# Kernel tuning notes

Hardware: AMD Instinct MI355X
Metric: run time of the kernel (lower is better)

Reference implementation:

```python
import jax, jax.numpy as jnp
import numpy as np

N_QUBITS = 12
N_LAYERS = 2
PATCH = 16
NPS = 14  # patches per side for 224/16
N_PATCHES = NPS * NPS
SCALE = 1.0 / np.sqrt(N_QUBITS)


def _butterfly_gates(n):
    # Faithful replication of QuantumOrthogonalLayer.butterfly_circuit indexing:
    # param_idx increments even when the (idx1, idx2) pair is skipped.
    gates, pidx = [], 0
    n_bl = int(np.ceil(np.log2(n)))
    for layer in range(n_bl):
        stride = 2 ** layer
        for start in range(0, n - stride, 2 * stride):
            for off in range(stride):
                i1, i2 = start + off, start + off + stride
                if i1 < n and i2 < n:
                    gates.append((pidx, i1, i2))
                pidx += 1
    nppl = sum(2 ** (n_bl - 1 - i) * 2 ** i for i in range(n_bl))  # n_params() = 32
    return gates, nppl

GATES, NPPL = _butterfly_gates(N_QUBITS)

# Pauli-Z sign table: qubit 0 is the most-significant bit of the flattened state index.
_bits = (np.arange(2 ** N_QUBITS)[:, None] >> np.arange(N_QUBITS - 1, -1, -1)[None, :]) & 1
Z_SIGNS = jnp.asarray(1.0 - 2.0 * _bits, dtype=jnp.float32)  # (4096, 12)


def _rbs_u(theta):
    # 4x4 real unitary of RY(2t,w1); CNOT(w1,w2); RY(-2t,w1); CNOT(w1,w2)
    c, s = jnp.cos(theta), jnp.sin(theta)
    c2, s2, cs = c * c, s * s, c * s
    return jnp.stack([
        jnp.stack([c2, s2, -cs, cs]),
        jnp.stack([s2, c2, cs, -cs]),
        jnp.stack([cs, -cs, c2, s2]),
        jnp.stack([-cs, cs, s2, c2]),
    ])


def _apply_2q(state, U, i, j):
    # state: (P, 2, 2, ..., 2); apply U to qubit axes i, j
    st = jnp.moveaxis(state, (1 + i, 1 + j), (-2, -1))
    shp = st.shape
    st = st.reshape(shp[:-2] + (4,)) @ U.T
    return jnp.moveaxis(st.reshape(shp), (-2, -1), (1 + i, 1 + j))


@jax.checkpoint
def quantum_expvals(features, params):
    # features: (P, n_qubits) angles; params: (N_LAYERS * NPPL,)
    P = features.shape[0]
    half = 0.5 * features
    amp = jnp.stack([jnp.cos(half), jnp.sin(half)], axis=-1)  # (P, n, 2) RY(x)|0>
    state = jnp.ones((P, 1), features.dtype)
    for q in range(N_QUBITS):  # product-state angle encoding
        state = (state[:, :, None] * amp[:, q][:, None, :]).reshape(P, -1)
    state = state.reshape((P,) + (2,) * N_QUBITS)
    for l in range(N_LAYERS):
        base = l * NPPL
        for pidx, w1, w2 in GATES:
            state = _apply_2q(state, _rbs_u(params[base + pidx]), w1, w2)
    probs = state.reshape(P, -1) ** 2
    return probs @ Z_SIGNS  # (P, n_qubits) <Z_i>


def setup_inputs() -> dict:
    key = jax.random.key(0)
    ks = jax.random.split(key, 6)
    x = jax.random.normal(ks[0], (4, 3, 224, 224), dtype=jnp.float32)
    W_proj = jax.random.normal(ks[1], (N_QUBITS, PATCH * PATCH), dtype=jnp.float32) / np.sqrt(PATCH * PATCH)
    b_proj = jnp.zeros((N_QUBITS,), jnp.float32)
    q_params = 0.1 * jax.random.normal(ks[2], (N_LAYERS * NPPL,), dtype=jnp.float32)
    k_params = 0.1 * jax.random.normal(ks[3], (N_LAYERS * NPPL,), dtype=jnp.float32)
    v_params = 0.1 * jax.random.normal(ks[4], (N_LAYERS * NPPL,), dtype=jnp.float32)
    W_cls = jax.random.normal(ks[5], (1000, N_PATCHES * N_QUBITS), dtype=jnp.float32) / np.sqrt(N_PATCHES * N_QUBITS)
    b_cls = jnp.zeros((1000,), jnp.float32)
    return {"x": x, "W_proj": W_proj, "b_proj": b_proj, "q_params": q_params,
            "k_params": k_params, "v_params": v_params, "W_cls": W_cls, "b_cls": b_cls}


def reference(x, W_proj, b_proj, q_params, k_params, v_params, W_cls, b_cls):
    B = x.shape[0]
    xg = jnp.mean(x, axis=1)  # channel average -> (B, H, W)
    patches = xg.reshape(B, NPS, PATCH, NPS, PATCH).transpose(0, 1, 3, 2, 4)
    patches = patches.reshape(B, N_PATCHES, PATCH * PATCH)
    proj = patches @ W_proj.T + b_proj  # (B, n_patches, n_qubits)
    feats = proj.reshape(-1, N_QUBITS)
    Q = quantum_expvals(feats, q_params).reshape(B, N_PATCHES, N_QUBITS)
    K = quantum_expvals(feats, k_params).reshape(B, N_PATCHES, N_QUBITS)
    V = quantum_expvals(feats, v_params).reshape(B, N_PATCHES, N_QUBITS)
    attn = jax.nn.softmax(jnp.einsum('bqd,bkd->bqk', Q, K) * SCALE, axis=-1)
    out = jnp.einsum('bqk,bkd->bqd', attn, V)  # (B, n_patches, n_qubits)
    logits = out.reshape(B, -1) @ W_cls.T + b_cls
    return logits
```

## Files before the change

kernel.cpp:

```cpp
#include <hip/hip_runtime.h>
#include <math.h>

#define NQ        12
#define NPS       14
#define NPATCH    196
#define NB        4
#define NCLS      1000
#define FEATDIM   2352
#define SCALE_F   0.28867513459481287f

typedef float v2f __attribute__((ext_vector_type(2)));

constexpr int PRa[8][5] = {
    {2,3,0,1, 4},
    {2,3,4,5, 6},
    {2,3,5,6, 7},
    {2,3,0,4, 6},
    {2,3,8,9,10},
    {2,3,9,10,11},
    {2,3,0,8,10},
    {2,3,1,5, 9},
};
constexpr int PTa[8][7] = {
    {5,6,7,8,9,10,11},
    {7,0,1,8,9,10,11},
    {0,1,4,8,9,10,11},
    {8,9,10,1,5,7,11},
    {4,0,1,5,6,7,11},
    {0,1,8,5,6,7,4},
    {1,5,9,6,7,11,4},
    {6,0,11,7,8,10,4},
};
constexpr bool BARa[8] = {false,false,false,false,true,false,false,true};

constexpr int cwgt(int X, int q) {
    for (int k = 0; k < 5; ++k) if (PRa[X][k] == q) return 1 << k;
    for (int m = 0; m < 7; ++m) if (PTa[X][m] == q) return 36 << m;
    return 0;
}
constexpr int rimmB(int X, int Y, int a) {
    int s = 0;
    for (int j = 0; j < 3; ++j)
        if ((a >> j) & 1) s += cwgt(X, PRa[Y][2 + j]);
    return s;
}

template<int TI>
__device__ __forceinline__ void relayoutB(v2f amp2[16], float* lds, int tid, int base) {
    constexpr int X = TI, Y = (TI + 1) & 7;
    float4* dst = (float4*)(lds + 36 * tid);
    #pragma unroll
    for (int k = 0; k < 8; ++k)
        dst[k] = make_float4(amp2[2*k][0], amp2[2*k][1], amp2[2*k+1][0], amp2[2*k+1][1]);
    if (BARa[TI]) __syncthreads();
    #pragma unroll
    for (int a = 0; a < 8; ++a) {
        float4 v = *(const float4*)(lds + base + rimmB(X, Y, a));
        amp2[2*a][0] = v.x; amp2[2*a][1] = v.y;
        amp2[2*a+1][0] = v.z; amp2[2*a+1][1] = v.w;
    }
    if (BARa[TI]) __syncthreads();
}

template<int MI, int MJ>
__device__ __forceinline__ void pk_gate(v2f a[16], float gc, float gs) {
    v2f H = {0.5f, 0.5f}, C = {gc, gc}, S = {gs, gs};
    #pragma unroll
    for (int m = 0; m < 16; ++m) {
        if (m & (MI | MJ)) continue;
        v2f a0 = a[m], a1 = a[m | MJ], a2 = a[m | MI], a3 = a[m | MI | MJ];
        v2f p  = a0 + a1, q  = a0 - a1;
        v2f p2 = a2 + a3, q2 = a2 - a3;
        v2f t1 = H * p  + C * q  - S * q2;
        v2f t2 = H * p2 + C * q2 + S * q;
        a[m]           = t1;
        a[m | MJ]      = p  - t1;
        a[m | MI]      = t2;
        a[m | MI | MJ] = p2 - t2;
    }
}

template<int MI, int MJ>
__device__ __forceinline__ void sc_gate(float* amp, float gc, float gs) {
    #pragma unroll
    for (int m = 0; m < 32; ++m) {
        if (m & (MI | MJ)) continue;
        float a0 = amp[m], a1 = amp[m | MJ], a2 = amp[m | MI], a3 = amp[m | MI | MJ];
        float p  = a0 + a1, q  = a0 - a1;
        float p2 = a2 + a3, q2 = a2 - a3;
        float t1 = 0.5f * p  + gc * q  - gs * q2;
        float t2 = 0.5f * p2 + gc * q2 + gs * q;
        amp[m]           = t1;
        amp[m | MJ]      = p  - t1;
        amp[m | MI]      = t2;
        amp[m | MI | MJ] = p2 - t2;
    }
}

template<int CTRL>
__device__ __forceinline__ float dppadd(float x) {
    int s = __builtin_amdgcn_update_dpp(0, __float_as_int(x), CTRL, 0xf, 0xf, true);
    return x + __int_as_float(s);
}
__device__ __forceinline__ float wave_sum(float x) {
    x = dppadd<0x111>(x);
    x = dppadd<0x112>(x);
    x = dppadd<0x114>(x);
    x = dppadd<0x118>(x);
    x = dppadd<0x142>(x);
    x = dppadd<0x143>(x);
    return x;
}

__global__ __launch_bounds__(128, 4) void qcirc_kernel(
    const float* __restrict__ x,
    const float* __restrict__ Wp,
    const float* __restrict__ bproj,
    const float* __restrict__ qp,
    const float* __restrict__ kp,
    const float* __restrict__ vp,
    float* __restrict__ qkv)
{
    __shared__ __align__(16) float lds[4608];
    __shared__ float chs[NQ], shs[NQ];
    __shared__ float gC[40], gS[40];
    __shared__ float red2[2][12];

    const int tid = threadIdx.x;
    const int p = blockIdx.x, b = blockIdx.y, c = blockIdx.z;
    const int bp = b * NPATCH + p;
    const float* params = (c == 0) ? qp : (c == 1) ? kp : vp;
    const int lane = tid & 63, wv = tid >> 6;

    float part[NQ];
    #pragma unroll
    for (int q = 0; q < NQ; ++q) part[q] = 0.0f;
    {
        int py = p / NPS, px = p % NPS;
        const float* xb = x + (size_t)b * 3 * 224 * 224;
        #pragma unroll
        for (int k = 0; k < 2; ++k) {
            int pix = tid + 128 * k;
            int off = (py * 16 + (pix >> 4)) * 224 + px * 16 + (pix & 15);
            float v = (xb[off] + xb[off + 50176] + xb[off + 100352]) * (1.0f / 3.0f);
            #pragma unroll
            for (int q = 0; q < NQ; ++q) part[q] += v * Wp[q * 256 + pix];
        }
    }
    if (tid < 40) {
        int l = tid / 20, g = tid - l * 20;
        float th = params[l * 32 + g];
        gC[tid] = 0.5f * cosf(2.0f * th);
        gS[tid] = 0.5f * sinf(2.0f * th);
    }
    #pragma unroll
    for (int q = 0; q < NQ; ++q) part[q] = wave_sum(part[q]);
    if (lane == 63) {
        #pragma unroll
        for (int q = 0; q < NQ; ++q) red2[wv][q] = part[q];
    }
    __syncthreads();
    if (tid < NQ) {
        float h = 0.5f * (red2[0][tid] + red2[1][tid] + bproj[tid]);
        chs[tid] = cosf(h); shs[tid] = sinf(h);
    }
    __syncthreads();

    int baseT[8];
    #pragma unroll
    for (int TI = 0; TI < 8; ++TI) {
        int Y = (TI + 1) & 7, s = 0;
        #pragma unroll
        for (int j = 0; j < 7; ++j)
            s += ((tid >> j) & 1) ? cwgt(TI, PTa[Y][j]) : 0;
        baseT[TI] = s;
    }

    v2f amp2[16];
    float* amp = (float*)amp2;
    {
        float hi = ((tid &  1) ? shs[5]  : chs[5])  *
                   ((tid &  2) ? shs[6]  : chs[6])  *
                   ((tid &  4) ? shs[7]  : chs[7])  *
                   ((tid &  8) ? shs[8]  : chs[8])  *
                   ((tid & 16) ? shs[9]  : chs[9])  *
                   ((tid & 32) ? shs[10] : chs[10]) *
                   ((tid & 64) ? shs[11] : chs[11]);
        float pA[8], pB[4];
        #pragma unroll
        for (int i = 0; i < 8; ++i)
            pA[i] = ((i & 1) ? shs[2] : chs[2]) * ((i & 2) ? shs[3] : chs[3]) *
                    ((i & 4) ? shs[0] : chs[0]);
        #pragma unroll
        for (int i = 0; i < 4; ++i)
            pB[i] = ((i & 1) ? shs[1] : chs[1]) * ((i & 2) ? shs[4] : chs[4]);
        #pragma unroll
        for (int r = 0; r < 32; ++r) amp[r] = pA[r & 7] * pB[r >> 3] * hi;
    }

    #pragma unroll 1
    for (int l = 0; l < 2; ++l) {
        const int bb = l * 20;
        pk_gate<2, 4>(amp2, gC[bb+0], gS[bb+0]);
        sc_gate<1, 2>(amp,  gC[bb+1], gS[bb+1]);
        sc_gate<4, 1>(amp,  gC[bb+6], gS[bb+6]);
        pk_gate<4, 1>(amp2, gC[bb+7], gS[bb+7]);
        relayoutB<0>(amp2, lds, tid, baseT[0]);
        pk_gate<2, 4>(amp2, gC[bb+2], gS[bb+2]);
        relayoutB<1>(amp2, lds, tid, baseT[1]);
        pk_gate<4, 8>(amp2, gC[bb+3],  gS[bb+3]);
        pk_gate<2, 8>(amp2, gC[bb+9],  gS[bb+9]);
        pk_gate<1, 8>(amp2, gC[bb+15], gS[bb+15]);
        relayoutB<2>(amp2, lds, tid, baseT[2]);
        pk_gate<4, 8>(amp2, gC[bb+8],  gS[bb+8]);
        pk_gate<2, 4>(amp2, gC[bb+12], gS[bb+12]);
        sc_gate<1,16>(amp,  gC[bb+14], gS[bb+14]);
        relayoutB<3>(amp2, lds, tid, baseT[3]);
        pk_gate<2, 4>(amp2, gC[bb+4], gS[bb+4]);
        relayoutB<4>(amp2, lds, tid, baseT[4]);
        pk_gate<4, 8>(amp2, gC[bb+5],  gS[bb+5]);
        pk_gate<2, 8>(amp2, gC[bb+11], gS[bb+11]);
        pk_gate<1, 8>(amp2, gC[bb+19], gS[bb+19]);
        relayoutB<5>(amp2, lds, tid, baseT[5]);
        pk_gate<4, 8>(amp2, gC[bb+10], gS[bb+10]);
        pk_gate<2, 4>(amp2, gC[bb+16], gS[bb+16]);
        sc_gate<1,16>(amp,  gC[bb+18], gS[bb+18]);
        relayoutB<6>(amp2, lds, tid, baseT[6]);
        pk_gate<2, 4>(amp2, gC[bb+13], gS[bb+13]);
        pk_gate<2, 8>(amp2, gC[bb+17], gS[bb+17]);
        if (l == 0) relayoutB<7>(amp2, lds, tid, baseT[7]);
    }

    float T, Sq2, Sq3, Sq1, Sq5, Sq9;
    {
        float t1[16]; Sq2 = 0.0f;
        #pragma unroll
        for (int i = 0; i < 16; ++i) {
            float e = amp[2*i] * amp[2*i], o = amp[2*i+1] * amp[2*i+1];
            t1[i] = e + o; Sq2 += e - o;
        }
        float t2[8]; Sq3 = 0.0f;
        #pragma unroll
        for (int i = 0; i < 8; ++i) { t2[i] = t1[2*i] + t1[2*i+1]; Sq3 += t1[2*i] - t1[2*i+1]; }
        float t3[4]; Sq1 = 0.0f;
        #pragma unroll
        for (int i = 0; i < 4; ++i) { t3[i] = t2[2*i] + t2[2*i+1]; Sq1 += t2[2*i] - t2[2*i+1]; }
        float t4[2]; Sq5 = 0.0f;
        #pragma unroll
        for (int i = 0; i < 2; ++i) { t4[i] = t3[2*i] + t3[2*i+1]; Sq5 += t3[2*i] - t3[2*i+1]; }
        T = t4[0] + t4[1]; Sq9 = t4[0] - t4[1];
    }
    float Vq6  = (tid &  1) ? -T : T;
    float Vq0  = (tid &  2) ? -T : T;
    float Vq11 = (tid &  4) ? -T : T;
    float Vq7  = (tid &  8) ? -T : T;
    float Vq8  = (tid & 16) ? -T : T;
    float Vq10 = (tid & 32) ? -T : T;
    T    = wave_sum(T);
    Vq6  = wave_sum(Vq6);  Vq0  = wave_sum(Vq0);  Vq11 = wave_sum(Vq11);
    Vq7  = wave_sum(Vq7);  Vq8  = wave_sum(Vq8);  Vq10 = wave_sum(Vq10);
    Sq2  = wave_sum(Sq2);  Sq3  = wave_sum(Sq3);  Sq1  = wave_sum(Sq1);
    Sq5  = wave_sum(Sq5);  Sq9  = wave_sum(Sq9);
    if (lane == 63) {
        red2[wv][0]  = Vq0;  red2[wv][1]  = Sq1;  red2[wv][2]  = Sq2;
        red2[wv][3]  = Sq3;  red2[wv][4]  = T;    red2[wv][5]  = Sq5;
        red2[wv][6]  = Vq6;  red2[wv][7]  = Vq7;  red2[wv][8]  = Vq8;
        red2[wv][9]  = Sq9;  red2[wv][10] = Vq10; red2[wv][11] = Vq11;
    }
    __syncthreads();
    if (tid < NQ) {
        float v1 = red2[1][tid];
        float s = red2[0][tid] + ((tid == 4) ? -v1 : v1);
        qkv[((size_t)c * (NB * NPATCH) + bp) * NQ + tid] = s;
    }
}

__global__ __launch_bounds__(256) void attn_kernel(
    const float* __restrict__ qkv,
    float* __restrict__ outb)
{
    int tid = threadIdx.x;
    int qp = blockIdx.x, b = blockIdx.y;
    const float* Q = qkv;
    const float* K = qkv + NB * NPATCH * NQ;
    const float* V = qkv + 2 * NB * NPATCH * NQ;

    __shared__ float redm[4], reds[4], redv[4][NQ];

    float4 q0 = ((const float4*)(Q + (b * NPATCH + qp) * NQ))[0];
    float4 q1 = ((const float4*)(Q + (b * NPATCH + qp) * NQ))[1];
    float4 q2 = ((const float4*)(Q + (b * NPATCH + qp) * NQ))[2];

    float score = -1e30f;
    float4 v0, v1, v2;
    if (tid < NPATCH) {
        const float4* K4 = (const float4*)(K + (b * NPATCH + tid) * NQ);
        float4 k0 = K4[0], k1 = K4[1], k2 = K4[2];
        float s = q0.x*k0.x + q0.y*k0.y + q0.z*k0.z + q0.w*k0.w
                + q1.x*k1.x + q1.y*k1.y + q1.z*k1.z + q1.w*k1.w
                + q2.x*k2.x + q2.y*k2.y + q2.z*k2.z + q2.w*k2.w;
        score = s * SCALE_F;
        const float4* V4 = (const float4*)(V + (b * NPATCH + tid) * NQ);
        v0 = V4[0]; v1 = V4[1]; v2 = V4[2];
    }
    float m = score;
    #pragma unroll
    for (int o = 32; o > 0; o >>= 1) m = fmaxf(m, __shfl_down(m, o));
    int lane = tid & 63, wv = tid >> 6;
    if (lane == 0) redm[wv] = m;
    __syncthreads();
    float maxv = fmaxf(fmaxf(redm[0], redm[1]), fmaxf(redm[2], redm[3]));

    float w = (tid < NPATCH) ? expf(score - maxv) : 0.0f;
    float sm = w;
    #pragma unroll
    for (int o = 32; o > 0; o >>= 1) sm += __shfl_down(sm, o);
    if (lane == 0) reds[wv] = sm;

    float part[NQ];
    #pragma unroll
    for (int d = 0; d < NQ; d++) part[d] = 0.0f;
    if (tid < NPATCH) {
        part[0] = w*v0.x; part[1] = w*v0.y; part[2]  = w*v0.z; part[3]  = w*v0.w;
        part[4] = w*v1.x; part[5] = w*v1.y; part[6]  = w*v1.z; part[7]  = w*v1.w;
        part[8] = w*v2.x; part[9] = w*v2.y; part[10] = w*v2.z; part[11] = w*v2.w;
    }
    #pragma unroll
    for (int d = 0; d < NQ; d++) {
        #pragma unroll
        for (int o = 32; o > 0; o >>= 1) part[d] += __shfl_down(part[d], o);
    }
    if (lane == 0) {
        #pragma unroll
        for (int d = 0; d < NQ; d++) redv[wv][d] = part[d];
    }
    __syncthreads();
    if (tid < NQ) {
        float sumv = reds[0] + reds[1] + reds[2] + reds[3];
        float s = redv[0][tid] + redv[1][tid] + redv[2][tid] + redv[3][tid];
        outb[(size_t)b * FEATDIM + qp * NQ + tid] = s / sumv;
    }
}

__global__ __launch_bounds__(256) void cls_kernel(
    const float* __restrict__ outb,
    const float* __restrict__ Wc,
    const float* __restrict__ bc,
    float* __restrict__ logits)
{
    int o = blockIdx.x, tid = threadIdx.x;
    float acc[NB] = {0.0f, 0.0f, 0.0f, 0.0f};
    const float4* w4 = (const float4*)(Wc + (size_t)o * FEATDIM);
    for (int j = tid; j < FEATDIM / 4; j += 256) {
        float4 w = w4[j];
        #pragma unroll
        for (int b = 0; b < NB; b++) {
            float4 ov = ((const float4*)(outb + (size_t)b * FEATDIM))[j];
            acc[b] += w.x*ov.x + w.y*ov.y + w.z*ov.z + w.w*ov.w;
        }
    }
    #pragma unroll
    for (int b = 0; b < NB; b++) {
        #pragma unroll
        for (int off = 32; off > 0; off >>= 1) acc[b] += __shfl_down(acc[b], off);
    }
    __shared__ float red[4][NB];
    int lane = tid & 63, wv = tid >> 6;
    if (lane == 0) {
        #pragma unroll
        for (int b = 0; b < NB; b++) red[wv][b] = acc[b];
    }
    __syncthreads();
    if (tid < NB) {
        float s = red[0][tid] + red[1][tid] + red[2][tid] + red[3][tid];
        logits[(size_t)tid * NCLS + o] = s + bc[o];
    }
}

extern "C" void kernel_launch(void* const* d_in, const int* in_sizes, int n_in,
                              void* d_out, int out_size, void* d_ws, size_t ws_size,
                              hipStream_t stream) {
    const float* x     = (const float*)d_in[0];
    const float* Wp    = (const float*)d_in[1];
    const float* bproj = (const float*)d_in[2];
    const float* qp    = (const float*)d_in[3];
    const float* kp    = (const float*)d_in[4];
    const float* vp    = (const float*)d_in[5];
    const float* Wc    = (const float*)d_in[6];
    const float* bc    = (const float*)d_in[7];
    float* logits = (float*)d_out;

    float* ws   = (float*)d_ws;
    float* qkv  = ws;
    float* outb = ws + 28224;

    qcirc_kernel<<<dim3(NPATCH, NB, 3), 128, 0, stream>>>(x, Wp, bproj, qp, kp, vp, qkv);
    attn_kernel <<<dim3(NPATCH, NB),    256, 0, stream>>>(qkv, outb);
    cls_kernel  <<<NCLS,                256, 0, stream>>>(outb, Wc, bc, logits);
}
```

Baseline: 116.5 us.

## Simulate Q, K, V circuits in one block sharing projection and interleaved stages

Merges the three per-parameter-set circuit blocks into one block per patch. The patch load and projection are now done once instead of three times, and the three state vectors are evolved together with their stages interleaved so each one's LDS relayout can overlap the others' gate math. The cost is three times the amplitude registers per thread, which removes the occupancy hint and may cause spills. The grid also shrinks to a third of its size, cutting parallelism to 784 blocks.

```diff
diff --git a/kernel.cpp b/kernel.cpp
--- a/kernel.cpp
+++ b/kernel.cpp
@@ -103,134 +103,34 @@
     return x + __int_as_float(s);
 }
 __device__ __forceinline__ float wave_sum(float x) {
-    x = dppadd<0x111>(x);
-    x = dppadd<0x112>(x);
-    x = dppadd<0x114>(x);
-    x = dppadd<0x118>(x);
-    x = dppadd<0x142>(x);
-    x = dppadd<0x143>(x);
+    x = dppadd<0x111>(x); x = dppadd<0x112>(x); x = dppadd<0x114>(x);
+    x = dppadd<0x118>(x); x = dppadd<0x142>(x); x = dppadd<0x143>(x);
     return x;
 }
 
-__global__ __launch_bounds__(128, 4) void qcirc_kernel(
-    const float* __restrict__ x,
-    const float* __restrict__ Wp,
-    const float* __restrict__ bproj,
-    const float* __restrict__ qp,
-    const float* __restrict__ kp,
-    const float* __restrict__ vp,
-    float* __restrict__ qkv)
-{
-    __shared__ __align__(16) float lds[4608];
-    __shared__ float chs[NQ], shs[NQ];
-    __shared__ float gC[40], gS[40];
-    __shared__ float red2[2][12];
-
-    const int tid = threadIdx.x;
-    const int p = blockIdx.x, b = blockIdx.y, c = blockIdx.z;
-    const int bp = b * NPATCH + p;
-    const float* params = (c == 0) ? qp : (c == 1) ? kp : vp;
-    const int lane = tid & 63, wv = tid >> 6;
-
-    float part[NQ];
-    #pragma unroll
-    for (int q = 0; q < NQ; ++q) part[q] = 0.0f;
-    {
-        int py = p / NPS, px = p % NPS;
-        const float* xb = x + (size_t)b * 3 * 224 * 224;
-        #pragma unroll
-        for (int k = 0; k < 2; ++k) {
-            int pix = tid + 128 * k;
-            int off = (py * 16 + (pix >> 4)) * 224 + px * 16 + (pix & 15);
-            float v = (xb[off] + xb[off + 50176] + xb[off + 100352]) * (1.0f / 3.0f);
-            #pragma unroll
-            for (int q = 0; q < NQ; ++q) part[q] += v * Wp[q * 256 + pix];
-        }
-    }
-    if (tid < 40) {
-        int l = tid / 20, g = tid - l * 20;
-        float th = params[l * 32 + g];
-        gC[tid] = 0.5f * cosf(2.0f * th);
-        gS[tid] = 0.5f * sinf(2.0f * th);
-    }
-    #pragma unroll
-    for (int q = 0; q < NQ; ++q) part[q] = wave_sum(part[q]);
-    if (lane == 63) {
-        #pragma unroll
-        for (int q = 0; q < NQ; ++q) red2[wv][q] = part[q];
-    }
-    __syncthreads();
-    if (tid < NQ) {
-        float h = 0.5f * (red2[0][tid] + red2[1][tid] + bproj[tid]);
-        chs[tid] = cosf(h); shs[tid] = sinf(h);
-    }
-    __syncthreads();
-
-    int baseT[8];
-    #pragma unroll
-    for (int TI = 0; TI < 8; ++TI) {
-        int Y = (TI + 1) & 7, s = 0;
-        #pragma unroll
-        for (int j = 0; j < 7; ++j)
-            s += ((tid >> j) & 1) ? cwgt(TI, PTa[Y][j]) : 0;
-        baseT[TI] = s;
-    }
-
-    v2f amp2[16];
-    float* amp = (float*)amp2;
-    {
-        float hi = ((tid &  1) ? shs[5]  : chs[5])  *
-                   ((tid &  2) ? shs[6]  : chs[6])  *
-                   ((tid &  4) ? shs[7]  : chs[7])  *
-                   ((tid &  8) ? shs[8]  : chs[8])  *
-                   ((tid & 16) ? shs[9]  : chs[9])  *
-                   ((tid & 32) ? shs[10] : chs[10]) *
-                   ((tid & 64) ? shs[11] : chs[11]);
-        float pA[8], pB[4];
-        #pragma unroll
-        for (int i = 0; i < 8; ++i)
-            pA[i] = ((i & 1) ? shs[2] : chs[2]) * ((i & 2) ? shs[3] : chs[3]) *
-                    ((i & 4) ? shs[0] : chs[0]);
-        #pragma unroll
-        for (int i = 0; i < 4; ++i)
-            pB[i] = ((i & 1) ? shs[1] : chs[1]) * ((i & 2) ? shs[4] : chs[4]);
-        #pragma unroll
-        for (int r = 0; r < 32; ++r) amp[r] = pA[r & 7] * pB[r >> 3] * hi;
-    }
-
-    #pragma unroll 1
-    for (int l = 0; l < 2; ++l) {
-        const int bb = l * 20;
-        pk_gate<2, 4>(amp2, gC[bb+0], gS[bb+0]);
-        sc_gate<1, 2>(amp,  gC[bb+1], gS[bb+1]);
-        sc_gate<4, 1>(amp,  gC[bb+6], gS[bb+6]);
-        pk_gate<4, 1>(amp2, gC[bb+7], gS[bb+7]);
-        relayoutB<0>(amp2, lds, tid, baseT[0]);
-        pk_gate<2, 4>(amp2, gC[bb+2], gS[bb+2]);
-        relayoutB<1>(amp2, lds, tid, baseT[1]);
-        pk_gate<4, 8>(amp2, gC[bb+3],  gS[bb+3]);
-        pk_gate<2, 8>(amp2, gC[bb+9],  gS[bb+9]);
-        pk_gate<1, 8>(amp2, gC[bb+15], gS[bb+15]);
-        relayoutB<2>(amp2, lds, tid, baseT[2]);
-        pk_gate<4, 8>(amp2, gC[bb+8],  gS[bb+8]);
-        pk_gate<2, 4>(amp2, gC[bb+12], gS[bb+12]);
-        sc_gate<1,16>(amp,  gC[bb+14], gS[bb+14]);
-        relayoutB<3>(amp2, lds, tid, baseT[3]);
-        pk_gate<2, 4>(amp2, gC[bb+4], gS[bb+4]);
-        relayoutB<4>(amp2, lds, tid, baseT[4]);
-        pk_gate<4, 8>(amp2, gC[bb+5],  gS[bb+5]);
-        pk_gate<2, 8>(amp2, gC[bb+11], gS[bb+11]);
-        pk_gate<1, 8>(amp2, gC[bb+19], gS[bb+19]);
-        relayoutB<5>(amp2, lds, tid, baseT[5]);
-        pk_gate<4, 8>(amp2, gC[bb+10], gS[bb+10]);
-        pk_gate<2, 4>(amp2, gC[bb+16], gS[bb+16]);
-        sc_gate<1,16>(amp,  gC[bb+18], gS[bb+18]);
-        relayoutB<6>(amp2, lds, tid, baseT[6]);
-        pk_gate<2, 4>(amp2, gC[bb+13], gS[bb+13]);
-        pk_gate<2, 8>(amp2, gC[bb+17], gS[bb+17]);
-        if (l == 0) relayoutB<7>(amp2, lds, tid, baseT[7]);
-    }
-
+#define RUN_S1(A2,A,O) pk_gate<2,4>(A2,gC[(O)+bb+0],gS[(O)+bb+0]); \
+    sc_gate<1,2>(A,gC[(O)+bb+1],gS[(O)+bb+1]); \
+    sc_gate<4,1>(A,gC[(O)+bb+6],gS[(O)+bb+6]); \
+    pk_gate<4,1>(A2,gC[(O)+bb+7],gS[(O)+bb+7]);
+#define RUN_S2(A2,A,O) pk_gate<2,4>(A2,gC[(O)+bb+2],gS[(O)+bb+2]);
+#define RUN_S3(A2,A,O) pk_gate<4,8>(A2,gC[(O)+bb+3],gS[(O)+bb+3]); \
+    pk_gate<2,8>(A2,gC[(O)+bb+9],gS[(O)+bb+9]); \
+    pk_gate<1,8>(A2,gC[(O)+bb+15],gS[(O)+bb+15]);
+#define RUN_S4(A2,A,O) pk_gate<4,8>(A2,gC[(O)+bb+8],gS[(O)+bb+8]); \
+    pk_gate<2,4>(A2,gC[(O)+bb+12],gS[(O)+bb+12]); \
+    sc_gate<1,16>(A,gC[(O)+bb+14],gS[(O)+bb+14]);
+#define RUN_S5(A2,A,O) pk_gate<2,4>(A2,gC[(O)+bb+4],gS[(O)+bb+4]);
+#define RUN_S6(A2,A,O) pk_gate<4,8>(A2,gC[(O)+bb+5],gS[(O)+bb+5]); \
+    pk_gate<2,8>(A2,gC[(O)+bb+11],gS[(O)+bb+11]); \
+    pk_gate<1,8>(A2,gC[(O)+bb+19],gS[(O)+bb+19]);
+#define RUN_S7(A2,A,O) pk_gate<4,8>(A2,gC[(O)+bb+10],gS[(O)+bb+10]); \
+    pk_gate<2,4>(A2,gC[(O)+bb+16],gS[(O)+bb+16]); \
+    sc_gate<1,16>(A,gC[(O)+bb+18],gS[(O)+bb+18]);
+#define RUN_S8(A2,A,O) pk_gate<2,4>(A2,gC[(O)+bb+13],gS[(O)+bb+13]); \
+    pk_gate<2,8>(A2,gC[(O)+bb+17],gS[(O)+bb+17]);
+
+__device__ __forceinline__ void expvals(const float* amp, int tid, int lane, int wv,
+                                        float red2[2][36], int coff) {
     float T, Sq2, Sq3, Sq1, Sq5, Sq9;
     {
         float t1[16]; Sq2 = 0.0f;
@@ -262,16 +162,146 @@
     Sq2  = wave_sum(Sq2);  Sq3  = wave_sum(Sq3);  Sq1  = wave_sum(Sq1);
     Sq5  = wave_sum(Sq5);  Sq9  = wave_sum(Sq9);
     if (lane == 63) {
-        red2[wv][0]  = Vq0;  red2[wv][1]  = Sq1;  red2[wv][2]  = Sq2;
-        red2[wv][3]  = Sq3;  red2[wv][4]  = T;    red2[wv][5]  = Sq5;
-        red2[wv][6]  = Vq6;  red2[wv][7]  = Vq7;  red2[wv][8]  = Vq8;
-        red2[wv][9]  = Sq9;  red2[wv][10] = Vq10; red2[wv][11] = Vq11;
+        float* r = &red2[wv][coff];
+        r[0] = Vq0;  r[1] = Sq1;  r[2]  = Sq2;  r[3]  = Sq3;
+        r[4] = T;    r[5] = Sq5;  r[6]  = Vq6;  r[7]  = Vq7;
+        r[8] = Vq8;  r[9] = Sq9;  r[10] = Vq10; r[11] = Vq11;
+    }
+}
+
+__global__ __launch_bounds__(128) void qcirc_kernel(
+    const float* __restrict__ x,
+    const float* __restrict__ Wp,
+    const float* __restrict__ bproj,
+    const float* __restrict__ qp,
+    const float* __restrict__ kp,
+    const float* __restrict__ vp,
+    float* __restrict__ qkv)
+{
+    __shared__ __align__(16) float lds[4608];
+    __shared__ float chs[NQ], shs[NQ];
+    __shared__ float gC[120], gS[120];
+    __shared__ float red2[2][36];
+
+    const int tid = threadIdx.x;
+    const int p = blockIdx.x, b = blockIdx.y;
+    const int bp = b * NPATCH + p;
+    const int lane = tid & 63, wv = tid >> 6;
+
+    float part[NQ];
+    #pragma unroll
+    for (int q = 0; q < NQ; ++q) part[q] = 0.0f;
+    {
+        int py = p / NPS, px = p % NPS;
+        const float* xb = x + (size_t)b * 3 * 224 * 224;
+        #pragma unroll
+        for (int k = 0; k < 2; ++k) {
+            int pix = tid + 128 * k;
+            int off = (py * 16 + (pix >> 4)) * 224 + px * 16 + (pix & 15);
+            float v = (xb[off] + xb[off + 50176] + xb[off + 100352]) * (1.0f / 3.0f);
+            #pragma unroll
+            for (int q = 0; q < NQ; ++q) part[q] += v * Wp[q * 256 + pix];
+        }
+    }
+    if (tid < 120) {
+        int c = tid / 40, r = tid - c * 40;
+        int l = r / 20, g = r - l * 20;
+        const float* pp = (c == 0) ? qp : (c == 1) ? kp : vp;
+        float th = pp[l * 32 + g];
+        gC[tid] = 0.5f * cosf(2.0f * th);
+        gS[tid] = 0.5f * sinf(2.0f * th);
+    }
+    #pragma unroll
+    for (int q = 0; q < NQ; ++q) part[q] = wave_sum(part[q]);
+    if (lane == 63) {
+        #pragma unroll
+        for (int q = 0; q < NQ; ++q) red2[wv][q] = part[q];
     }
     __syncthreads();
     if (tid < NQ) {
+        float h = 0.5f * (red2[0][tid] + red2[1][tid] + bproj[tid]);
+        chs[tid] = cosf(h); shs[tid] = sinf(h);
+    }
+    __syncthreads();
+
+    int baseT[8];
+    #pragma unroll
+    for (int TI = 0; TI < 8; ++TI) {
+        int Y = (TI + 1) & 7, s = 0;
+        #pragma unroll
+        for (int j = 0; j < 7; ++j)
+            s += ((tid >> j) & 1) ? cwgt(TI, PTa[Y][j]) : 0;
+        baseT[TI] = s;
+    }
+
+    v2f A2[16], B2[16], C2[16];
+    float* fA = (float*)A2; float* fB = (float*)B2; float* fC = (float*)C2;
+    {
+        float hi = ((tid &  1) ? shs[5]  : chs[5])  *
+                   ((tid &  2) ? shs[6]  : chs[6])  *
+                   ((tid &  4) ? shs[7]  : chs[7])  *
+                   ((tid &  8) ? shs[8]  : chs[8])  *
+                   ((tid & 16) ? shs[9]  : chs[9])  *
+                   ((tid & 32) ? shs[10] : chs[10]) *
+                   ((tid & 64) ? shs[11] : chs[11]);
+        float pA[8], pB[4];
+        #pragma unroll
+        for (int i = 0; i < 8; ++i)
+            pA[i] = ((i & 1) ? shs[2] : chs[2]) * ((i & 2) ? shs[3] : chs[3]) *
+                    ((i & 4) ? shs[0] : chs[0]);
+        #pragma unroll
+        for (int i = 0; i < 4; ++i)
+            pB[i] = ((i & 1) ? shs[1] : chs[1]) * ((i & 2) ? shs[4] : chs[4]);
+        #pragma unroll
+        for (int r = 0; r < 32; ++r) {
+            float v = pA[r & 7] * pB[r >> 3] * hi;
+            fA[r] = v; fB[r] = v; fC[r] = v;
+        }
+    }
+
+    #pragma unroll 1
+    for (int l = 0; l < 2; ++l) {
+        const int bb = l * 20;
+        RUN_S1(A2, fA, 0)  relayoutB<0>(A2, lds, tid, baseT[0]);
+        RUN_S1(B2, fB, 40) relayoutB<0>(B2, lds, tid, baseT[0]);
+        RUN_S1(C2, fC, 80) relayoutB<0>(C2, lds, tid, baseT[0]);
+        RUN_S2(A2, fA, 0)  relayoutB<1>(A2, lds, tid, baseT[1]);
+        RUN_S2(B2, fB, 40) relayoutB<1>(B2, lds, tid, baseT[1]);
+        RUN_S2(C2, fC, 80) relayoutB<1>(C2, lds, tid, baseT[1]);
+        RUN_S3(A2, fA, 0)  relayoutB<2>(A2, lds, tid, baseT[2]);
+        RUN_S3(B2, fB, 40) relayoutB<2>(B2, lds, tid, baseT[2]);
+        RUN_S3(C2, fC, 80) relayoutB<2>(C2, lds, tid, baseT[2]);
+        RUN_S4(A2, fA, 0)  relayoutB<3>(A2, lds, tid, baseT[3]);
+        RUN_S4(B2, fB, 40) relayoutB<3>(B2, lds, tid, baseT[3]);
+        RUN_S4(C2, fC, 80) relayoutB<3>(C2, lds, tid, baseT[3]);
+        RUN_S5(A2, fA, 0)  relayoutB<4>(A2, lds, tid, baseT[4]);
+        RUN_S5(B2, fB, 40) relayoutB<4>(B2, lds, tid, baseT[4]);
+        RUN_S5(C2, fC, 80) relayoutB<4>(C2, lds, tid, baseT[4]);
+        RUN_S6(A2, fA, 0)  relayoutB<5>(A2, lds, tid, baseT[5]);
+        RUN_S6(B2, fB, 40) relayoutB<5>(B2, lds, tid, baseT[5]);
+        RUN_S6(C2, fC, 80) relayoutB<5>(C2, lds, tid, baseT[5]);
+        RUN_S7(A2, fA, 0)  relayoutB<6>(A2, lds, tid, baseT[6]);
+        RUN_S7(B2, fB, 40) relayoutB<6>(B2, lds, tid, baseT[6]);
+        RUN_S7(C2, fC, 80) relayoutB<6>(C2, lds, tid, baseT[6]);
+        RUN_S8(A2, fA, 0)
+        RUN_S8(B2, fB, 40)
+        RUN_S8(C2, fC, 80)
+        if (l == 0) {
+            relayoutB<7>(A2, lds, tid, baseT[7]);
+            relayoutB<7>(B2, lds, tid, baseT[7]);
+            relayoutB<7>(C2, lds, tid, baseT[7]);
+        }
+    }
+
+    expvals(fA, tid, lane, wv, red2, 0);
+    expvals(fB, tid, lane, wv, red2, 12);
+    expvals(fC, tid, lane, wv, red2, 24);
+    __syncthreads();
+    if (tid < 36) {
+        int c = tid / 12, q = tid - c * 12;
         float v1 = red2[1][tid];
-        float s = red2[0][tid] + ((tid == 4) ? -v1 : v1);
-        qkv[((size_t)c * (NB * NPATCH) + bp) * NQ + tid] = s;
+        float s = red2[0][tid] + ((q == 4) ? -v1 : v1);
+        qkv[((size_t)c * (NB * NPATCH) + bp) * NQ + q] = s;
     }
 }
 
@@ -394,7 +424,7 @@
     float* qkv  = ws;
     float* outb = ws + 28224;
 
-    qcirc_kernel<<<dim3(NPATCH, NB, 3), 128, 0, stream>>>(x, Wp, bproj, qp, kp, vp, qkv);
-    attn_kernel <<<dim3(NPATCH, NB),    256, 0, stream>>>(qkv, outb);
-    cls_kernel  <<<NCLS,                256, 0, stream>>>(outb, Wc, bc, logits);
-}
+    qcirc_kernel<<<dim3(NPATCH, NB), 128, 0, stream>>>(x, Wp, bproj, qp, kp, vp, qkv);
+    attn_kernel <<<dim3(NPATCH, NB), 256, 0, stream>>>(qkv, outb);
+    cls_kernel  <<<NCLS,             256, 0, stream>>>(outb, Wc, bc, logits);
+}
```

After: 127.6 us. +9.6%, slower.
